# Kernel tuning notes

Measured on AMD Instinct MI355X. Metric: run time of the kernel, lower is better.

## Reference

```python
import jax, jax.numpy as jnp
import numpy as np

D_MODEL = 64
N_HEADS = 4
D_HEAD = D_MODEL // N_HEADS
LN_EPS = 1e-5


def setup_inputs() -> dict:
    key = jax.random.key(0)
    ks = jax.random.split(key, 10)
    d = D_MODEL
    s = 1.0 / np.sqrt(d)
    X = jax.random.normal(ks[0], (4, 256, 200, d), dtype=jnp.float32)
    Wq = jax.random.uniform(ks[1], (d, d), jnp.float32, -s, s)
    bq = jax.random.uniform(ks[2], (d,), jnp.float32, -s, s)
    Wk = jax.random.uniform(ks[3], (d, d), jnp.float32, -s, s)
    bk = jax.random.uniform(ks[4], (d,), jnp.float32, -s, s)
    Wv = jax.random.uniform(ks[5], (d, d), jnp.float32, -s, s)
    bv = jax.random.uniform(ks[6], (d,), jnp.float32, -s, s)
    Wo = jax.random.uniform(ks[7], (d, d), jnp.float32, -s, s)
    bo = jax.random.uniform(ks[8], (d,), jnp.float32, -s, s)
    gamma = jnp.ones((d,), jnp.float32)
    beta = jnp.zeros((d,), jnp.float32)
    return {"X": X, "Wq": Wq, "bq": bq, "Wk": Wk, "bk": bk,
            "Wv": Wv, "bv": bv, "Wo": Wo, "bo": bo,
            "gamma": gamma, "beta": beta}


def reference(X, Wq, bq, Wk, bk, Wv, bv, Wo, bo, gamma, beta):
    B, T, N, d = X.shape
    H, dh = N_HEADS, D_HEAD
    # [B, T, N, d] -> [B*N, T, d]
    Xbn = jnp.transpose(X, (0, 2, 1, 3)).reshape(B * N, T, d)
    Q = Xbn @ Wq + bq
    K = Xbn @ Wk + bk
    V = Xbn @ Wv + bv

    def split(x):  # [BN, T, d] -> [BN, H, T, dh]
        return jnp.transpose(x.reshape(B * N, T, H, dh), (0, 2, 1, 3))

    Qh, Kh, Vh = split(Q), split(K), split(V)
    scores = jnp.einsum('bhtd,bhsd->bhts', Qh, Kh) / np.sqrt(dh).astype(np.float32)
    attn = jax.nn.softmax(scores, axis=-1)  # dropout is identity at eval
    out_h = jnp.einsum('bhts,bhsd->bhtd', attn, Vh)
    out = jnp.transpose(out_h, (0, 2, 1, 3)).reshape(B * N, T, d)
    out = out @ Wo + bo
    out = out + Xbn
    # LayerNorm over last dim
    mu = jnp.mean(out, axis=-1, keepdims=True)
    var = jnp.var(out, axis=-1, keepdims=True)
    out = (out - mu) * jax.lax.rsqrt(var + LN_EPS) * gamma + beta
    # [B*N, T, d] -> [B, T, N, d]
    return jnp.transpose(out.reshape(B, N, T, d), (0, 2, 1, 3))
```

## Files before the change

### kernel.cpp

```cpp
#include <hip/hip_runtime.h>
#include <hip/hip_bf16.h>
#include <hip/hip_fp8.h>

constexpr int B_ = 4, T_ = 256, N_ = 200, D_ = 64, H_ = 4;
constexpr int BN_ = B_ * N_;
constexpr float LN_EPS = 1e-5f;
constexpr float QSCALE = 0.25f * 1.4426950408889634f;

typedef short short8_t __attribute__((ext_vector_type(8)));
typedef float f32x4 __attribute__((ext_vector_type(4)));

#if __has_builtin(__builtin_amdgcn_exp2f)
#define EXP2(x) __builtin_amdgcn_exp2f(x)
#else
#define EXP2(x) exp2f(x)
#endif

constexpr int OFF_K  = 16384;
constexpr int OFF_V  = 32768;
constexpr int OFF_WO = 36864;
constexpr int ARENA_BYTES = 50176;

__device__ __forceinline__ ushort f2bf(float f) {
    union { float f; unsigned u; } v; v.f = f;
    unsigned u = v.u + 0x7FFFu + ((v.u >> 16) & 1u);
    return (ushort)(u >> 16);
}

template <bool HI>
__device__ __forceinline__ unsigned cvt2fp8(float a, float b, unsigned old) {
#if __has_builtin(__builtin_amdgcn_cvt_pk_fp8_f32)
    return __builtin_amdgcn_cvt_pk_fp8_f32(a, b, old, HI);
#else
    __hip_fp8_e4m3 fa(a), fb(b);
    unsigned v = (unsigned)fa.__x | ((unsigned)fb.__x << 8);
    return HI ? ((old & 0x0000FFFFu) | (v << 16)) : ((old & 0xFFFF0000u) | v);
#endif
}

__device__ __forceinline__ f32x4 mfma_fp8(long long a, long long b, f32x4 c) {
    return __builtin_amdgcn_mfma_f32_16x16x32_fp8_fp8(a, b, c, 0, 0, 0);
}
__device__ __forceinline__ f32x4 mfma_bf16(short8_t a, short8_t b, f32x4 c) {
    return __builtin_amdgcn_mfma_f32_16x16x32_bf16(a, b, c, 0, 0, 0);
}

__global__ __launch_bounds__(512, 6) void fused_attn_kernel(
    const float* __restrict__ X,
    const float* __restrict__ Wq, const float* __restrict__ bq,
    const float* __restrict__ Wk, const float* __restrict__ bk,
    const float* __restrict__ Wv, const float* __restrict__ bv,
    const float* __restrict__ Wo, const float* __restrict__ bo,
    const float* __restrict__ gamma, const float* __restrict__ beta,
    float* __restrict__ out)
{
    __shared__ __align__(16) unsigned char arena[ARENA_BYTES];
    unsigned char* Qf8 = arena;
    unsigned char* Kf8 = arena + OFF_K;
    unsigned char* Vf8 = arena + OFF_V;
    ushort* sWT   = (ushort*)arena;
    ushort* sAttn = (ushort*)arena;
    ushort* sWoT  = (ushort*)(arena + OFF_WO);

    const int bn   = blockIdx.x;
    const int b    = bn / N_;
    const int n    = bn - b * N_;
    const int tid  = threadIdx.x;
    const int lane = tid & 63;
    const int w    = tid >> 6;
    const int lm   = lane & 15;
    const int g    = lane >> 4;
    const int wbase = w * 32;

    const f32x4 zz = {0.f, 0.f, 0.f, 0.f};

    short8_t af[2][2];
    #pragma unroll
    for (int mt = 0; mt < 2; ++mt) {
        #pragma unroll
        for (int kf = 0; kf < 2; ++kf) {
            const int t = wbase + mt * 16 + lm;
            const float* xp = X + (((long)(b * T_ + t)) * N_ + n) * D_ + kf * 32 + 8 * g;
            const float4 x0 = *(const float4*)xp;
            const float4 x1 = *(const float4*)(xp + 4);
            union { short8_t v; unsigned u[4]; } tmp;
            tmp.u[0] = ((unsigned)f2bf(x0.y) << 16) | f2bf(x0.x);
            tmp.u[1] = ((unsigned)f2bf(x0.w) << 16) | f2bf(x0.z);
            tmp.u[2] = ((unsigned)f2bf(x1.y) << 16) | f2bf(x1.x);
            tmp.u[3] = ((unsigned)f2bf(x1.w) << 16) | f2bf(x1.z);
            af[mt][kf] = tmp.v;
        }
    }

    const float* Wm[3] = {Wk, Wv, Wq};
    const float* bm[3] = {bk, bv, bq};
    #pragma unroll 1
    for (int m = 0; m < 3; ++m) {
        for (int idx = tid; idx < 2048; idx += 512) {
            const int c = idx & 63, kp = idx >> 6;
            const unsigned lo = f2bf(Wm[m][(2 * kp) * 64 + c]);
            const unsigned hi = f2bf(Wm[m][(2 * kp + 1) * 64 + c]);
            *(unsigned*)&sWT[c * 72 + 2 * kp] = lo | (hi << 16);
        }
        __syncthreads();

        if (m == 0) {
            #pragma unroll
            for (int dt = 0; dt < 4; ++dt) {
                const short8_t bf0 = *(const short8_t*)&sWT[(dt * 16 + lm) * 72 + 8 * g];
                const short8_t bf1 = *(const short8_t*)&sWT[(dt * 16 + lm) * 72 + 32 + 8 * g];
                const float4 bI = *(const float4*)(bm[0] + dt * 16 + 4 * g);
                #pragma unroll
                for (int q2 = 0; q2 < 2; ++q2) {
                    f32x4 acc = mfma_bf16(bf0, af[q2][0], zz);
                    acc = mfma_bf16(bf1, af[q2][1], acc);
                    unsigned pk = cvt2fp8<false>(acc[0] + bI.x, acc[1] + bI.y, 0u);
                    pk = cvt2fp8<true>(acc[2] + bI.z, acc[3] + bI.w, pk);
                    *(unsigned*)(Kf8 + dt * 4096 + (wbase + q2 * 16 + lm) * 16 + 4 * g) = pk;
                }
            }
            __syncthreads();
        } else if (m == 1) {
            #pragma unroll
            for (int nt = 0; nt < 4; ++nt) {
                const short8_t bf0 = *(const short8_t*)&sWT[(nt * 16 + lm) * 72 + 8 * g];
                const short8_t bf1 = *(const short8_t*)&sWT[(nt * 16 + lm) * 72 + 32 + 8 * g];
                const float blv = bm[1][nt * 16 + lm];
                #pragma unroll
                for (int mt = 0; mt < 2; ++mt) {
                    f32x4 acc = mfma_bf16(af[mt][0], bf0, zz);
                    acc = mfma_bf16(af[mt][1], bf1, acc);
                    unsigned pk = cvt2fp8<false>(acc[0] + blv, acc[1] + blv, 0u);
                    pk = cvt2fp8<true>(acc[2] + blv, acc[3] + blv, pk);
                    *(unsigned*)(Vf8 + (nt * 16 + lm) * 272 + wbase + mt * 16 + 4 * g) = pk;
                }
            }
            __syncthreads();
        } else {
            short8_t bfq[4][2];
            #pragma unroll
            for (int dt = 0; dt < 4; ++dt) {
                bfq[dt][0] = *(const short8_t*)&sWT[(dt * 16 + lm) * 72 + 8 * g];
                bfq[dt][1] = *(const short8_t*)&sWT[(dt * 16 + lm) * 72 + 32 + 8 * g];
            }
            __syncthreads();
            #pragma unroll
            for (int dt = 0; dt < 4; ++dt) {
                const float4 bI = *(const float4*)(bm[2] + dt * 16 + 4 * g);
                #pragma unroll
                for (int q2 = 0; q2 < 2; ++q2) {
                    f32x4 acc = mfma_bf16(bfq[dt][0], af[q2][0], zz);
                    acc = mfma_bf16(bfq[dt][1], af[q2][1], acc);
                    unsigned pk = cvt2fp8<false>((acc[0] + bI.x) * QSCALE,
                                                 (acc[1] + bI.y) * QSCALE, 0u);
                    pk = cvt2fp8<true>((acc[2] + bI.z) * QSCALE,
                                       (acc[3] + bI.w) * QSCALE, pk);
                    *(unsigned*)(Qf8 + dt * 4096 + (wbase + q2 * 16 + lm) * 16 + 4 * g) = pk;
                }
            }
            __syncthreads();
        }
    }

    const int h     = w >> 1;
    const int qbase = (w & 1) * 128;
    const bool glo  = (g < 2);

    f32x4 oacc[4];
    float lsum[4];
    float inv[4];
    unsigned pend[8];

    #pragma unroll 1
    for (int pass = 0; pass < 2; ++pass) {
        const int qoff = qbase + pass * 64;
        long long qf[4];
        #pragma unroll
        for (int qt = 0; qt < 4; ++qt)
            qf[qt] = glo ? *(const long long*)(Qf8 + h * 4096 + (qoff + qt * 16 + lm) * 16 + 8 * g)
                         : 0ll;
        #pragma unroll
        for (int qt = 0; qt < 4; ++qt) { oacc[qt] = zz; lsum[qt] = 0.f; }

        #pragma unroll 1
        for (int c = 0; c < 8; ++c) {
            const long long kfe = glo ? *(const long long*)(Kf8 + h * 4096 + ((2 * c) * 16 + lm) * 16 + 8 * g) : 0ll;
            const long long kfo = glo ? *(const long long*)(Kf8 + h * 4096 + ((2 * c + 1) * 16 + lm) * 16 + 8 * g) : 0ll;
            const unsigned va = *(const unsigned*)(Vf8 + (h * 16 + lm) * 272 + 32 * c + 4 * g);
            const unsigned vb = *(const unsigned*)(Vf8 + (h * 16 + lm) * 272 + 32 * c + 16 + 4 * g);
            const long long vf = (long long)(((unsigned long long)vb << 32) | va);

            #pragma unroll
            for (int qt = 0; qt < 4; ++qt) {
                const f32x4 se = mfma_fp8(kfe, qf[qt], zz);
                const f32x4 so = mfma_fp8(kfo, qf[qt], zz);
                const float pe0 = EXP2(se[0]), pe1 = EXP2(se[1]);
                const float pe2 = EXP2(se[2]), pe3 = EXP2(se[3]);
                const float po0 = EXP2(so[0]), po1 = EXP2(so[1]);
                const float po2 = EXP2(so[2]), po3 = EXP2(so[3]);
                lsum[qt] += ((pe0 + pe1) + (pe2 + pe3)) + ((po0 + po1) + (po2 + po3));
                unsigned a0 = cvt2fp8<false>(pe0, pe1, 0u); a0 = cvt2fp8<true>(pe2, pe3, a0);
                unsigned a1 = cvt2fp8<false>(po0, po1, 0u); a1 = cvt2fp8<true>(po2, po3, a1);
                const long long pa = (long long)(((unsigned long long)a1 << 32) | a0);
                oacc[qt] = mfma_fp8(pa, vf, oacc[qt]);
            }
        }

        #pragma unroll
        for (int qt = 0; qt < 4; ++qt) {
            float t0 = lsum[qt] + __shfl_xor(lsum[qt], 16, 64);
            t0 += __shfl_xor(t0, 32, 64);
            inv[qt] = 1.0f / t0;
        }

        if (pass == 0) {
            #pragma unroll
            for (int qt = 0; qt < 4; ++qt) {
                const float i0 = __shfl(inv[qt], 4 * g + 0, 64);
                const float i1 = __shfl(inv[qt], 4 * g + 1, 64);
                const float i2 = __shfl(inv[qt], 4 * g + 2, 64);
                const float i3 = __shfl(inv[qt], 4 * g + 3, 64);
                pend[2 * qt]     = ((unsigned)f2bf(oacc[qt][1] * i1) << 16) | f2bf(oacc[qt][0] * i0);
                pend[2 * qt + 1] = ((unsigned)f2bf(oacc[qt][3] * i3) << 16) | f2bf(oacc[qt][2] * i2);
            }
        }
    }

    __syncthreads();

    #pragma unroll
    for (int qt = 0; qt < 4; ++qt) {
        const int row0 = qbase + qt * 16 + 4 * g;
        sAttn[(row0 + 0) * 72 + h * 16 + lm] = (ushort)(pend[2 * qt] & 0xFFFFu);
        sAttn[(row0 + 1) * 72 + h * 16 + lm] = (ushort)(pend[2 * qt] >> 16);
        sAttn[(row0 + 2) * 72 + h * 16 + lm] = (ushort)(pend[2 * qt + 1] & 0xFFFFu);
        sAttn[(row0 + 3) * 72 + h * 16 + lm] = (ushort)(pend[2 * qt + 1] >> 16);
    }
    #pragma unroll
    for (int qt = 0; qt < 4; ++qt)
        #pragma unroll
        for (int r = 0; r < 4; ++r) {
            const float iv = __shfl(inv[qt], 4 * g + r, 64);
            sAttn[(qbase + 64 + qt * 16 + 4 * g + r) * 72 + h * 16 + lm] = f2bf(oacc[qt][r] * iv);
        }
    for (int idx = tid; idx < 2048; idx += 512) {
        const int c = idx & 63, kp = idx >> 6;
        const unsigned lo = f2bf(Wo[(2 * kp) * 64 + c]);
        const unsigned hi = f2bf(Wo[(2 * kp + 1) * 64 + c]);
        *(unsigned*)&sWoT[c * 72 + 2 * kp] = lo | (hi << 16);
    }

    __syncthreads();

    short8_t aF[2][2];
    #pragma unroll
    for (int mt = 0; mt < 2; ++mt)
        #pragma unroll
        for (int kf = 0; kf < 2; ++kf)
            aF[mt][kf] = *(const short8_t*)&sAttn[(wbase + mt * 16 + lm) * 72 + kf * 32 + 8 * g];

    f32x4 acc2[2][4];
    #pragma unroll
    for (int nt = 0; nt < 4; ++nt) {
        const short8_t wf0 = *(const short8_t*)&sWoT[(nt * 16 + lm) * 72 + 8 * g];
        const short8_t wf1 = *(const short8_t*)&sWoT[(nt * 16 + lm) * 72 + 32 + 8 * g];
        #pragma unroll
        for (int mt = 0; mt < 2; ++mt) {
            acc2[mt][nt] = mfma_bf16(aF[mt][0], wf0, zz);
            acc2[mt][nt] = mfma_bf16(aF[mt][1], wf1, acc2[mt][nt]);
        }
    }

    float bo_l[4], ga_l[4], be_l[4];
    #pragma unroll
    for (int nt = 0; nt < 4; ++nt) {
        bo_l[nt] = bo[nt * 16 + lm];
        ga_l[nt] = gamma[nt * 16 + lm];
        be_l[nt] = beta[nt * 16 + lm];
    }

    #pragma unroll
    for (int mt = 0; mt < 2; ++mt)
        #pragma unroll
        for (int r = 0; r < 4; ++r) {
            const int t = wbase + mt * 16 + 4 * g + r;
            const long base = (((long)(b * T_ + t)) * N_ + n) * D_;
            float v[4];
            #pragma unroll
            for (int nt = 0; nt < 4; ++nt)
                v[nt] = acc2[mt][nt][r] + bo_l[nt] + X[base + nt * 16 + lm];
            float s1 = (v[0] + v[1]) + (v[2] + v[3]);
            float s2 = (v[0] * v[0] + v[1] * v[1]) + (v[2] * v[2] + v[3] * v[3]);
            #pragma unroll
            for (int m = 1; m <= 8; m <<= 1) {
                s1 += __shfl_xor(s1, m, 64);
                s2 += __shfl_xor(s2, m, 64);
            }
            const float mu  = s1 * 0.015625f;
            const float var = s2 * 0.015625f - mu * mu;
            const float rs  = rsqrtf(var + LN_EPS);
            #pragma unroll
            for (int nt = 0; nt < 4; ++nt)
                out[base + nt * 16 + lm] = (v[nt] - mu) * rs * ga_l[nt] + be_l[nt];
        }
}

extern "C" void kernel_launch(void* const* d_in, const int* in_sizes, int n_in,
                              void* d_out, int out_size, void* d_ws, size_t ws_size,
                              hipStream_t stream) {
    const float* X     = (const float*)d_in[0];
    const float* Wq    = (const float*)d_in[1];
    const float* bq    = (const float*)d_in[2];
    const float* Wk    = (const float*)d_in[3];
    const float* bk    = (const float*)d_in[4];
    const float* Wv    = (const float*)d_in[5];
    const float* bv    = (const float*)d_in[6];
    const float* Wo    = (const float*)d_in[7];
    const float* bo    = (const float*)d_in[8];
    const float* gamma = (const float*)d_in[9];
    const float* beta  = (const float*)d_in[10];

    fused_attn_kernel<<<BN_, 512, 0, stream>>>(
        X, Wq, bq, Wk, bk, Wv, bv, Wo, bo, gamma, beta, (float*)d_out);
}
```

Baseline: 80.65 us.

## Split fused attention into QKV projection and attention/output kernels via workspace

Splits the single fused kernel into two launches. The first projects Q, K and V to fp8 and writes them to a global workspace, with block 0 also writing a transposed bf16 copy of Wo. The second reads Q, K, V and Wo straight from global memory for attention, output projection and LayerNorm, and adds s_setprio around the MFMA loop. The aim is to shrink per-block LDS and raise occupancy, at the cost of extra global traffic (about 39 MB written and read back) and a second launch.

```diff
diff --git a/kernel.cpp b/kernel.cpp
--- a/kernel.cpp
+++ b/kernel.cpp
@@ -16,10 +16,10 @@
 #define EXP2(x) exp2f(x)
 #endif
 
-constexpr int OFF_K  = 16384;
-constexpr int OFF_V  = 32768;
-constexpr int OFF_WO = 36864;
-constexpr int ARENA_BYTES = 50176;
+constexpr size_t WS_Q  = 0;
+constexpr size_t WS_K  = 13107200;
+constexpr size_t WS_V  = 26214400;
+constexpr size_t WS_WO = 39321600;
 
 __device__ __forceinline__ ushort f2bf(float f) {
     union { float f; unsigned u; } v; v.f = f;
@@ -45,22 +45,15 @@
     return __builtin_amdgcn_mfma_f32_16x16x32_bf16(a, b, c, 0, 0, 0);
 }
 
-__global__ __launch_bounds__(512, 6) void fused_attn_kernel(
+__global__ __launch_bounds__(512, 4) void qkv_proj_kernel(
     const float* __restrict__ X,
     const float* __restrict__ Wq, const float* __restrict__ bq,
     const float* __restrict__ Wk, const float* __restrict__ bk,
     const float* __restrict__ Wv, const float* __restrict__ bv,
-    const float* __restrict__ Wo, const float* __restrict__ bo,
-    const float* __restrict__ gamma, const float* __restrict__ beta,
-    float* __restrict__ out)
+    const float* __restrict__ Wo,
+    unsigned char* __restrict__ ws)
 {
-    __shared__ __align__(16) unsigned char arena[ARENA_BYTES];
-    unsigned char* Qf8 = arena;
-    unsigned char* Kf8 = arena + OFF_K;
-    unsigned char* Vf8 = arena + OFF_V;
-    ushort* sWT   = (ushort*)arena;
-    ushort* sAttn = (ushort*)arena;
-    ushort* sWoT  = (ushort*)(arena + OFF_WO);
+    __shared__ __align__(16) ushort sWT[64 * 72];
 
     const int bn   = blockIdx.x;
     const int b    = bn / N_;
@@ -92,8 +85,8 @@
         }
     }
 
-    const float* Wm[3] = {Wk, Wv, Wq};
-    const float* bm[3] = {bk, bv, bq};
+    const float* Wm[3] = {Wq, Wk, Wv};
+    const float* bm[3] = {bq, bk, bv};
     #pragma unroll 1
     for (int m = 0; m < 3; ++m) {
         for (int idx = tid; idx < 2048; idx += 512) {
@@ -104,72 +97,83 @@
         }
         __syncthreads();
 
-        if (m == 0) {
+        if (m < 2) {
+            unsigned char* dst = ws + ((m == 0) ? WS_Q : WS_K) + (size_t)bn * 16384;
+            const float scl = (m == 0) ? QSCALE : 1.0f;
             #pragma unroll
             for (int dt = 0; dt < 4; ++dt) {
                 const short8_t bf0 = *(const short8_t*)&sWT[(dt * 16 + lm) * 72 + 8 * g];
                 const short8_t bf1 = *(const short8_t*)&sWT[(dt * 16 + lm) * 72 + 32 + 8 * g];
-                const float4 bI = *(const float4*)(bm[0] + dt * 16 + 4 * g);
+                const float4 bI = *(const float4*)(bm[m] + dt * 16 + 4 * g);
                 #pragma unroll
                 for (int q2 = 0; q2 < 2; ++q2) {
                     f32x4 acc = mfma_bf16(bf0, af[q2][0], zz);
                     acc = mfma_bf16(bf1, af[q2][1], acc);
-                    unsigned pk = cvt2fp8<false>(acc[0] + bI.x, acc[1] + bI.y, 0u);
-                    pk = cvt2fp8<true>(acc[2] + bI.z, acc[3] + bI.w, pk);
-                    *(unsigned*)(Kf8 + dt * 4096 + (wbase + q2 * 16 + lm) * 16 + 4 * g) = pk;
+                    unsigned pk = cvt2fp8<false>((acc[0] + bI.x) * scl, (acc[1] + bI.y) * scl, 0u);
+                    pk = cvt2fp8<true>((acc[2] + bI.z) * scl, (acc[3] + bI.w) * scl, pk);
+                    *(unsigned*)(dst + dt * 4096 + (wbase + q2 * 16 + lm) * 16 + 4 * g) = pk;
                 }
             }
-            __syncthreads();
-        } else if (m == 1) {
+        } else {
+            unsigned char* dst = ws + WS_V + (size_t)bn * 16384;
             #pragma unroll
             for (int nt = 0; nt < 4; ++nt) {
                 const short8_t bf0 = *(const short8_t*)&sWT[(nt * 16 + lm) * 72 + 8 * g];
                 const short8_t bf1 = *(const short8_t*)&sWT[(nt * 16 + lm) * 72 + 32 + 8 * g];
-                const float blv = bm[1][nt * 16 + lm];
+                const float blv = bm[2][nt * 16 + lm];
                 #pragma unroll
                 for (int mt = 0; mt < 2; ++mt) {
                     f32x4 acc = mfma_bf16(af[mt][0], bf0, zz);
                     acc = mfma_bf16(af[mt][1], bf1, acc);
                     unsigned pk = cvt2fp8<false>(acc[0] + blv, acc[1] + blv, 0u);
                     pk = cvt2fp8<true>(acc[2] + blv, acc[3] + blv, pk);
-                    *(unsigned*)(Vf8 + (nt * 16 + lm) * 272 + wbase + mt * 16 + 4 * g) = pk;
+                    *(unsigned*)(dst + (nt * 16 + lm) * 256 + wbase + mt * 16 + 4 * g) = pk;
                 }
             }
-            __syncthreads();
-        } else {
-            short8_t bfq[4][2];
-            #pragma unroll
-            for (int dt = 0; dt < 4; ++dt) {
-                bfq[dt][0] = *(const short8_t*)&sWT[(dt * 16 + lm) * 72 + 8 * g];
-                bfq[dt][1] = *(const short8_t*)&sWT[(dt * 16 + lm) * 72 + 32 + 8 * g];
-            }
-            __syncthreads();
-            #pragma unroll
-            for (int dt = 0; dt < 4; ++dt) {
-                const float4 bI = *(const float4*)(bm[2] + dt * 16 + 4 * g);
-                #pragma unroll
-                for (int q2 = 0; q2 < 2; ++q2) {
-                    f32x4 acc = mfma_bf16(bfq[dt][0], af[q2][0], zz);
-                    acc = mfma_bf16(bfq[dt][1], af[q2][1], acc);
-                    unsigned pk = cvt2fp8<false>((acc[0] + bI.x) * QSCALE,
-                                                 (acc[1] + bI.y) * QSCALE, 0u);
-                    pk = cvt2fp8<true>((acc[2] + bI.z) * QSCALE,
-                                       (acc[3] + bI.w) * QSCALE, pk);
-                    *(unsigned*)(Qf8 + dt * 4096 + (wbase + q2 * 16 + lm) * 16 + 4 * g) = pk;
-                }
-            }
-            __syncthreads();
-        }
-    }
+        }
+        __syncthreads();
+    }
+
+    if (bn == 0) {
+        ushort* wo = (ushort*)(ws + WS_WO);
+        for (int idx = tid; idx < 2048; idx += 512) {
+            const int c = idx & 63, kp = idx >> 6;
+            const unsigned lo = f2bf(Wo[(2 * kp) * 64 + c]);
+            const unsigned hi = f2bf(Wo[(2 * kp + 1) * 64 + c]);
+            *(unsigned*)&wo[c * 64 + 2 * kp] = lo | (hi << 16);
+        }
+    }
+}
+
+__global__ __launch_bounds__(512, 6) void attn_out_kernel(
+    const unsigned char* __restrict__ ws,
+    const float* __restrict__ X,
+    const float* __restrict__ bo,
+    const float* __restrict__ gamma, const float* __restrict__ beta,
+    float* __restrict__ out)
+{
+    __shared__ __align__(16) ushort sAttn[256 * 72];
+
+    const int bn   = blockIdx.x;
+    const int b    = bn / N_;
+    const int n    = bn - b * N_;
+    const int tid  = threadIdx.x;
+    const int lane = tid & 63;
+    const int w    = tid >> 6;
+    const int lm   = lane & 15;
+    const int g    = lane >> 4;
+    const int wbase = w * 32;
+
+    const f32x4 zz = {0.f, 0.f, 0.f, 0.f};
+
+    const unsigned char* Qg = ws + WS_Q + (size_t)bn * 16384;
+    const unsigned char* Kg = ws + WS_K + (size_t)bn * 16384;
+    const unsigned char* Vg = ws + WS_V + (size_t)bn * 16384;
+    const ushort* WoT = (const ushort*)(ws + WS_WO);
 
     const int h     = w >> 1;
     const int qbase = (w & 1) * 128;
     const bool glo  = (g < 2);
-
-    f32x4 oacc[4];
-    float lsum[4];
-    float inv[4];
-    unsigned pend[8];
 
     #pragma unroll 1
     for (int pass = 0; pass < 2; ++pass) {
@@ -177,19 +181,23 @@
         long long qf[4];
         #pragma unroll
         for (int qt = 0; qt < 4; ++qt)
-            qf[qt] = glo ? *(const long long*)(Qf8 + h * 4096 + (qoff + qt * 16 + lm) * 16 + 8 * g)
+            qf[qt] = glo ? *(const long long*)(Qg + h * 4096 + (qoff + qt * 16 + lm) * 16 + 8 * g)
                          : 0ll;
+
+        f32x4 oacc[4];
+        float lsum[4];
         #pragma unroll
         for (int qt = 0; qt < 4; ++qt) { oacc[qt] = zz; lsum[qt] = 0.f; }
 
         #pragma unroll 1
         for (int c = 0; c < 8; ++c) {
-            const long long kfe = glo ? *(const long long*)(Kf8 + h * 4096 + ((2 * c) * 16 + lm) * 16 + 8 * g) : 0ll;
-            const long long kfo = glo ? *(const long long*)(Kf8 + h * 4096 + ((2 * c + 1) * 16 + lm) * 16 + 8 * g) : 0ll;
-            const unsigned va = *(const unsigned*)(Vf8 + (h * 16 + lm) * 272 + 32 * c + 4 * g);
-            const unsigned vb = *(const unsigned*)(Vf8 + (h * 16 + lm) * 272 + 32 * c + 16 + 4 * g);
+            const long long kfe = glo ? *(const long long*)(Kg + h * 4096 + ((2 * c) * 16 + lm) * 16 + 8 * g) : 0ll;
+            const long long kfo = glo ? *(const long long*)(Kg + h * 4096 + ((2 * c + 1) * 16 + lm) * 16 + 8 * g) : 0ll;
+            const unsigned va = *(const unsigned*)(Vg + (h * 16 + lm) * 256 + 32 * c + 4 * g);
+            const unsigned vb = *(const unsigned*)(Vg + (h * 16 + lm) * 256 + 32 * c + 16 + 4 * g);
             const long long vf = (long long)(((unsigned long long)vb << 32) | va);
 
+            __builtin_amdgcn_s_setprio(1);
             #pragma unroll
             for (int qt = 0; qt < 4; ++qt) {
                 const f32x4 se = mfma_fp8(kfe, qf[qt], zz);
@@ -204,8 +212,10 @@
                 const long long pa = (long long)(((unsigned long long)a1 << 32) | a0);
                 oacc[qt] = mfma_fp8(pa, vf, oacc[qt]);
             }
-        }
-
+            __builtin_amdgcn_s_setprio(0);
+        }
+
+        float inv[4];
         #pragma unroll
         for (int qt = 0; qt < 4; ++qt) {
             float t0 = lsum[qt] + __shfl_xor(lsum[qt], 16, 64);
@@ -213,41 +223,13 @@
             inv[qt] = 1.0f / t0;
         }
 
-        if (pass == 0) {
-            #pragma unroll
-            for (int qt = 0; qt < 4; ++qt) {
-                const float i0 = __shfl(inv[qt], 4 * g + 0, 64);
-                const float i1 = __shfl(inv[qt], 4 * g + 1, 64);
-                const float i2 = __shfl(inv[qt], 4 * g + 2, 64);
-                const float i3 = __shfl(inv[qt], 4 * g + 3, 64);
-                pend[2 * qt]     = ((unsigned)f2bf(oacc[qt][1] * i1) << 16) | f2bf(oacc[qt][0] * i0);
-                pend[2 * qt + 1] = ((unsigned)f2bf(oacc[qt][3] * i3) << 16) | f2bf(oacc[qt][2] * i2);
-            }
-        }
-    }
-
-    __syncthreads();
-
-    #pragma unroll
-    for (int qt = 0; qt < 4; ++qt) {
-        const int row0 = qbase + qt * 16 + 4 * g;
-        sAttn[(row0 + 0) * 72 + h * 16 + lm] = (ushort)(pend[2 * qt] & 0xFFFFu);
-        sAttn[(row0 + 1) * 72 + h * 16 + lm] = (ushort)(pend[2 * qt] >> 16);
-        sAttn[(row0 + 2) * 72 + h * 16 + lm] = (ushort)(pend[2 * qt + 1] & 0xFFFFu);
-        sAttn[(row0 + 3) * 72 + h * 16 + lm] = (ushort)(pend[2 * qt + 1] >> 16);
-    }
-    #pragma unroll
-    for (int qt = 0; qt < 4; ++qt)
-        #pragma unroll
-        for (int r = 0; r < 4; ++r) {
-            const float iv = __shfl(inv[qt], 4 * g + r, 64);
-            sAttn[(qbase + 64 + qt * 16 + 4 * g + r) * 72 + h * 16 + lm] = f2bf(oacc[qt][r] * iv);
-        }
-    for (int idx = tid; idx < 2048; idx += 512) {
-        const int c = idx & 63, kp = idx >> 6;
-        const unsigned lo = f2bf(Wo[(2 * kp) * 64 + c]);
-        const unsigned hi = f2bf(Wo[(2 * kp + 1) * 64 + c]);
-        *(unsigned*)&sWoT[c * 72 + 2 * kp] = lo | (hi << 16);
+        #pragma unroll
+        for (int qt = 0; qt < 4; ++qt)
+            #pragma unroll
+            for (int r = 0; r < 4; ++r) {
+                const float iv = __shfl(inv[qt], 4 * g + r, 64);
+                sAttn[(qoff + qt * 16 + 4 * g + r) * 72 + h * 16 + lm] = f2bf(oacc[qt][r] * iv);
+            }
     }
 
     __syncthreads();
@@ -262,8 +244,8 @@
     f32x4 acc2[2][4];
     #pragma unroll
     for (int nt = 0; nt < 4; ++nt) {
-        const short8_t wf0 = *(const short8_t*)&sWoT[(nt * 16 + lm) * 72 + 8 * g];
-        const short8_t wf1 = *(const short8_t*)&sWoT[(nt * 16 + lm) * 72 + 32 + 8 * g];
+        const short8_t wf0 = *(const short8_t*)&WoT[(nt * 16 + lm) * 64 + 8 * g];
+        const short8_t wf1 = *(const short8_t*)&WoT[(nt * 16 + lm) * 64 + 32 + 8 * g];
         #pragma unroll
         for (int mt = 0; mt < 2; ++mt) {
             acc2[mt][nt] = mfma_bf16(aF[mt][0], wf0, zz);
@@ -320,6 +302,8 @@
     const float* gamma = (const float*)d_in[9];
     const float* beta  = (const float*)d_in[10];
 
-    fused_attn_kernel<<<BN_, 512, 0, stream>>>(
-        X, Wq, bq, Wk, bk, Wv, bv, Wo, bo, gamma, beta, (float*)d_out);
-}
+    unsigned char* ws = (unsigned char*)d_ws;
+
+    qkv_proj_kernel<<<BN_, 512, 0, stream>>>(X, Wq, bq, Wk, bk, Wv, bv, Wo, ws);
+    attn_out_kernel<<<BN_, 512, 0, stream>>>(ws, X, bo, gamma, beta, (float*)d_out);
+}
```

Result: slower. 105.7 us (+31.0%).
